# Optimization experiments

Hardware: AMD Instinct MI355X
Metric: run time of the kernel (lower is better)

The kernel has to match this reference:

```python
import jax, jax.numpy as jnp
import numpy as np

F, V, D, B = 3, 512, 8192, 64


def setup_inputs() -> dict:
    key = jax.random.key(0)
    k1, k2 = jax.random.split(key)
    # bipolar (MAP) codebooks: (f, v, d) in {-1, +1}
    codebooks = jnp.sign(jax.random.normal(k1, (F, V, D), dtype=jnp.float32))
    codebooks = jnp.where(codebooks == 0, 1.0, codebooks)
    # ground-truth factors -> inputs = bind (elementwise product) of one codevector per factor
    idx = jax.random.randint(k2, (B, F), 0, V)
    picked = codebooks[jnp.arange(F)[None, :], idx]          # (b, f, d)
    inputs = jnp.prod(picked, axis=1)                         # (b, d)
    # init estimates: bundle (superposition) of each codebook, signed, broadcast to batch
    init = jnp.sign(jnp.sum(codebooks, axis=1))               # (f, d)
    init = jnp.where(init == 0, 1.0, init)
    init_estimates = jnp.broadcast_to(init, (B, F, D)).astype(jnp.float32)
    return {"inputs": inputs, "init_estimates": init_estimates,
            "codebooks": codebooks, "iterations": 10}


def reference(inputs, init_estimates, codebooks, iterations):
    f = init_estimates.shape[-2]

    def step(est):
        # MAP inverse is identity; inv_others[:, j] = prod_{i != j} est[:, i]
        rolled = jnp.stack([jnp.roll(est, i, axis=-2) for i in range(1, f)], axis=-2)  # (b,f,f-1,d)
        inv_others = jnp.prod(rolled, axis=-2)                 # (b, f, d)  multibind
        new_est = inputs[:, None, :] * inv_others              # bind       (b, f, d)
        sim = jnp.einsum('bfd,fvd->bfv', new_est, codebooks)   # codebook similarity
        return jnp.sign(jnp.einsum('bfv,fvd->bfd', sim, codebooks))

    def cond(c):
        est, old, cnt, done = c
        return (cnt < iterations) & jnp.logical_not(done)

    def body(c):
        est, old, cnt, done = c
        new = step(est)
        done = jnp.all(new == old)
        return (new, new, cnt + 1, done)

    carry0 = (init_estimates, init_estimates, jnp.int32(0), jnp.array(False))
    est, _, cnt, _ = jax.lax.while_loop(cond, body, carry0)

    # cleanup: nearest codevector per factor (argmax dot similarity)
    sims = jnp.einsum('bfd,fvd->bfv', est, codebooks)
    outcome = jnp.argmax(sims, axis=-1)                        # (b, f) int indices
    return outcome, cnt - 1
```

## Files before the change

### kernel.cpp

```cpp
#include <hip/hip_runtime.h>

#define F 3
#define V 512
#define D 8192
#define B 64
#define ITERS 10

typedef __bf16 bf16_t;
typedef __bf16 bf16x8 __attribute__((ext_vector_type(8)));
typedef __bf16 bf16x4 __attribute__((ext_vector_type(4)));
typedef float f32x4 __attribute__((ext_vector_type(4)));

__global__ void k_init_small(const float* __restrict__ ie, bf16_t* __restrict__ est0,
                             float* __restrict__ simBase, int* __restrict__ anydiff) {
  long tid = (long)blockIdx.x * blockDim.x + threadIdx.x;
  long NT  = (long)gridDim.x * blockDim.x;
  for (long i = tid * 4; i < (long)B * F * D; i += NT * 4) {
    f32x4 x = *(const f32x4*)(ie + i);
    bf16x4 y;
    y[0] = (bf16_t)x[0]; y[1] = (bf16_t)x[1]; y[2] = (bf16_t)x[2]; y[3] = (bf16_t)x[3];
    *(bf16x4*)(est0 + i) = y;
  }
  f32x4 z = {0.f, 0.f, 0.f, 0.f};
  for (long i = tid * 4; i < (long)(ITERS + 1) * F * B * V; i += NT * 4)
    *(f32x4*)(simBase + i) = z;
  if (tid < 16) anydiff[tid] = 0;
}

__global__ __launch_bounds__(256) void k_init_cb(const float* __restrict__ Csrc,
                                                 bf16_t* __restrict__ Cb,
                                                 bf16_t* __restrict__ CbT) {
  int f = blockIdx.z, vt = blockIdx.y, dt = blockIdx.x;
  __shared__ bf16_t tile[64 * 65];
  int t = threadIdx.x;
  int v0 = vt * 64, d0 = dt * 64;
#pragma unroll
  for (int p = 0; p < 16; ++p) {
    int q = t + 256 * p;
    int i = q >> 6, j = q & 63;
    bf16_t x = (bf16_t)Csrc[((long)(f * V + v0 + i)) * D + d0 + j];
    tile[i * 65 + j] = x;
    Cb[((long)(f * V + v0 + i)) * D + d0 + j] = x;
  }
  __syncthreads();
#pragma unroll
  for (int p = 0; p < 16; ++p) {
    int q = t + 256 * p;
    int jj = q >> 6, ii = q & 63;
    CbT[((long)f * D + d0 + jj) * V + v0 + ii] = tile[ii * 65 + jj];
  }
}

__global__ __launch_bounds__(256) void k_sim(const float* __restrict__ inputs,
                                             const bf16_t* __restrict__ Cb,
                                             const bf16_t* __restrict__ est0,
                                             const bf16_t* __restrict__ est1,
                                             float* __restrict__ simBase,
                                             const int* __restrict__ anydiff, int iter) {
  const int f = blockIdx.z, vt = blockIdx.y, ks = blockIdx.x;
  const bf16_t* est;
  float* sim;
  const bool is_final = (iter >= ITERS);
  if (is_final) {
    int first0 = ITERS;
    for (int i = 0; i < ITERS; ++i)
      if (anydiff[i] == 0) { first0 = i; break; }
    int par = (first0 < ITERS) ? ((first0 + 1) & 1) : 0;
    est = par ? est1 : est0;
    sim = simBase + (long)ITERS * (F * B * V);
  } else {
    for (int i = 0; i < iter; ++i)
      if (anydiff[i] == 0) return;
    est = (iter & 1) ? est1 : est0;
    sim = simBase + (long)iter * (F * B * V);
  }
  const int f1 = (f + 1) % 3, f2 = (f + 2) % 3;

  __shared__ __attribute__((aligned(16))) bf16_t lA[64 * 136];

  const int t = threadIdx.x;
  const int lane = t & 63, w = t >> 6;
  const int lm = lane & 15, quad = lane >> 4;

  f32x4 zero = {0.f, 0.f, 0.f, 0.f};
  f32x4 acc[4];
#pragma unroll
  for (int mt = 0; mt < 4; ++mt) acc[mt] = zero;

  const int v0 = vt * 64;
  const int dbase = ks * 512;
  const bf16_t* bp = Cb + ((long)(f * V + v0 + w * 16 + lm)) * D + dbase;

  for (int c = 0; c < 4; ++c) {
    const int d0c = dbase + c * 128;
    __syncthreads();
#pragma unroll
    for (int p = 0; p < 4; ++p) {
      int q = t + 256 * p;
      int b = q >> 4, dd = (q & 15) * 8;
      if (is_final) {
        *(bf16x8*)&lA[b * 136 + dd] =
            *(const bf16x8*)(est + ((long)b * F + f) * D + d0c + dd);
      } else {
        const float* ip = inputs + (long)b * D + d0c + dd;
        f32x4 x0 = *(const f32x4*)ip;
        f32x4 x1 = *(const f32x4*)(ip + 4);
        bf16x8 e1 = *(const bf16x8*)(est + ((long)b * F + f1) * D + d0c + dd);
        bf16x8 e2 = *(const bf16x8*)(est + ((long)b * F + f2) * D + d0c + dd);
        bf16x8 o;
#pragma unroll
        for (int i = 0; i < 4; ++i) {
          o[i]     = (bf16_t)(x0[i] * (float)e1[i]     * (float)e2[i]);
          o[i + 4] = (bf16_t)(x1[i] * (float)e1[i + 4] * (float)e2[i + 4]);
        }
        *(bf16x8*)&lA[b * 136 + dd] = o;
      }
    }
    __syncthreads();
#pragma unroll
    for (int ks2 = 0; ks2 < 4; ++ks2) {
      const int kb = ks2 * 32 + quad * 8;
      bf16x8 bfrag = *(const bf16x8*)(bp + c * 128 + kb);
#pragma unroll
      for (int mt = 0; mt < 4; ++mt) {
        bf16x8 afrag = *(const bf16x8*)&lA[(mt * 16 + lm) * 136 + kb];
        acc[mt] = __builtin_amdgcn_mfma_f32_16x16x32_bf16(afrag, bfrag, acc[mt], 0, 0, 0);
      }
    }
  }
  const int v = v0 + w * 16 + lm;
#pragma unroll
  for (int mt = 0; mt < 4; ++mt)
#pragma unroll
    for (int r = 0; r < 4; ++r) {
      int b = mt * 16 + quad * 4 + r;
      atomicAdd(&sim[(f * B + b) * V + v], acc[mt][r]);
    }
}

__global__ __launch_bounds__(256) void k_upd(const float* __restrict__ simBase,
                                             const bf16_t* __restrict__ CbT,
                                             bf16_t* __restrict__ est0,
                                             bf16_t* __restrict__ est1,
                                             int* __restrict__ anydiff, int iter) {
  const int f = blockIdx.y;
  const int d0 = blockIdx.x * 64;
  for (int i = 0; i < iter; ++i)
    if (anydiff[i] == 0) return;
  const bf16_t* estIn = (iter & 1) ? est1 : est0;
  bf16_t* estOut = (iter & 1) ? est0 : est1;
  const float* sim = simBase + (long)iter * (F * B * V) + f * (B * V);

  __shared__ __attribute__((aligned(16))) bf16_t lAh[64 * 136];
  __shared__ __attribute__((aligned(16))) bf16_t lAl[64 * 136];

  const int t = threadIdx.x;
  const int lane = t & 63, w = t >> 6;
  const int lm = lane & 15, quad = lane >> 4;

  f32x4 zero = {0.f, 0.f, 0.f, 0.f};
  f32x4 accH[4], accL[4];
#pragma unroll
  for (int mt = 0; mt < 4; ++mt) { accH[mt] = zero; accL[mt] = zero; }

  const bf16_t* bp = CbT + ((long)f * D + d0 + w * 16 + lm) * V;

  for (int c = 0; c < 4; ++c) {
    const int vb = c * 128;
    __syncthreads();
#pragma unroll
    for (int p = 0; p < 4; ++p) {
      int q = t + 256 * p;
      int b = q >> 4, vv = (q & 15) * 8;
      const float* sp = sim + b * V + vb + vv;
      bf16x8 h, l;
#pragma unroll
      for (int i = 0; i < 8; ++i) {
        int si = (int)sp[i];
        h[i] = (bf16_t)(float)(si >> 8);
        l[i] = (bf16_t)(float)(si & 255);
      }
      *(bf16x8*)&lAh[b * 136 + vv] = h;
      *(bf16x8*)&lAl[b * 136 + vv] = l;
    }
    __syncthreads();
#pragma unroll
    for (int ks2 = 0; ks2 < 4; ++ks2) {
      const int kb = ks2 * 32 + quad * 8;
      bf16x8 bfrag = *(const bf16x8*)(bp + vb + kb);
#pragma unroll
      for (int mt = 0; mt < 4; ++mt) {
        bf16x8 ah = *(const bf16x8*)&lAh[(mt * 16 + lm) * 136 + kb];
        bf16x8 al = *(const bf16x8*)&lAl[(mt * 16 + lm) * 136 + kb];
        accH[mt] = __builtin_amdgcn_mfma_f32_16x16x32_bf16(ah, bfrag, accH[mt], 0, 0, 0);
        accL[mt] = __builtin_amdgcn_mfma_f32_16x16x32_bf16(al, bfrag, accL[mt], 0, 0, 0);
      }
    }
  }
  bool anyd = false;
  const int d = d0 + w * 16 + lm;
#pragma unroll
  for (int mt = 0; mt < 4; ++mt)
#pragma unroll
    for (int r = 0; r < 4; ++r) {
      int b = mt * 16 + quad * 4 + r;
      float val = 256.f * accH[mt][r] + accL[mt][r];
      float s = (val > 0.f) ? 1.f : ((val < 0.f) ? -1.f : 0.f);
      long idx = ((long)b * F + f) * D + d;
      estOut[idx] = (bf16_t)s;
      anyd |= ((float)estIn[idx] != s);
    }
  if (__any(anyd) && lane == 0) atomicOr(&anydiff[iter], 1);
}

__global__ __launch_bounds__(64) void k_out(const float* __restrict__ simBase,
                                            const int* __restrict__ anydiff,
                                            int* __restrict__ out) {
  const float* sim = simBase + (long)ITERS * (F * B * V);
  int bid = blockIdx.x;
  int b = bid / F, f = bid % F;
  int lane = threadIdx.x;
  const float* row = sim + (f * B + b) * V;
  float best = -1e30f;
  int bidx = 0;
#pragma unroll
  for (int i = 0; i < V / 64; ++i) {
    int v = lane + 64 * i;
    float x = row[v];
    if (x > best) { best = x; bidx = v; }
  }
  for (int off = 32; off; off >>= 1) {
    float ov = __shfl_down(best, off, 64);
    int oi = __shfl_down(bidx, off, 64);
    if (ov > best || (ov == best && oi < bidx)) { best = ov; bidx = oi; }
  }
  if (lane == 0) out[b * F + f] = bidx;
  if (bid == 0 && lane == 0) {
    int first0 = ITERS;
    for (int i = 0; i < ITERS; ++i)
      if (anydiff[i] == 0) { first0 = i; break; }
    int cnt = (first0 < ITERS) ? (first0 + 1) : ITERS;
    out[B * F] = cnt - 1;
  }
}

extern "C" void kernel_launch(void* const* d_in, const int* in_sizes, int n_in,
                              void* d_out, int out_size, void* d_ws, size_t ws_size,
                              hipStream_t stream) {
  const float* inputs    = (const float*)d_in[0];
  const float* init_est  = (const float*)d_in[1];
  const float* codebooks = (const float*)d_in[2];

  char* w = (char*)d_ws;
  size_t o = 0;
  auto alloc = [&](size_t bytes) -> void* {
    void* p = w + o;
    o = (o + bytes + 255) & ~(size_t)255;
    return p;
  };
  bf16_t* Cb   = (bf16_t*)alloc((size_t)F * V * D * 2);
  bf16_t* CbT  = (bf16_t*)alloc((size_t)F * D * V * 2);
  bf16_t* est0 = (bf16_t*)alloc((size_t)B * F * D * 2);
  bf16_t* est1 = (bf16_t*)alloc((size_t)B * F * D * 2);
  float* simBase = (float*)alloc((size_t)(ITERS + 1) * F * B * V * 4);
  int* anydiff = (int*)alloc(64);

  k_init_small<<<1024, 256, 0, stream>>>(init_est, est0, simBase, anydiff);
  k_init_cb<<<dim3(128, 8, 3), 256, 0, stream>>>(codebooks, Cb, CbT);

  for (int j = 0; j < ITERS; ++j) {
    k_sim<<<dim3(16, 8, 3), 256, 0, stream>>>(inputs, Cb, est0, est1, simBase, anydiff, j);
    k_upd<<<dim3(128, 3), 256, 0, stream>>>(simBase, CbT, est0, est1, anydiff, j);
  }
  k_sim<<<dim3(16, 8, 3), 256, 0, stream>>>(inputs, Cb, est0, est1, simBase, anydiff, ITERS);
  k_out<<<B * F, 64, 0, stream>>>(simBase, anydiff, (int*)d_out);
}
```

Before: 621.0 us.

## Fuse iteration loop into one persistent kernel with software grid barrier

Replaces the 22 separate per-iteration sim/update launches and the final argmax kernel with one persistent 384-block kernel that uses an atomic-counter grid barrier between phases. Sim buffers shrink to a two-slot ring, with each slot re-zeroed inside the loop, and convergence is checked in-kernel so all blocks break out together. This removes kernel launch overhead and the early-return checks on anydiff. In exchange it relies on all 384 blocks being co-resident (two per CU via launch bounds), and spinning barriers add latency at each phase boundary.

Measured after the change: 1.582 ms. 155% more time.

```diff
diff --git a/kernel.cpp b/kernel.cpp
--- a/kernel.cpp
+++ b/kernel.cpp
@@ -5,14 +5,33 @@
 #define D 8192
 #define B 64
 #define ITERS 10
+#define NBLK 384
+#define SIMN (F * B * V)
 
 typedef __bf16 bf16_t;
 typedef __bf16 bf16x8 __attribute__((ext_vector_type(8)));
 typedef __bf16 bf16x4 __attribute__((ext_vector_type(4)));
 typedef float f32x4 __attribute__((ext_vector_type(4)));
 
+__device__ inline void gridbar(int* cnt, int* gen) {
+  __syncthreads();
+  if (threadIdx.x == 0) {
+    int g = __hip_atomic_load(gen, __ATOMIC_RELAXED, __HIP_MEMORY_SCOPE_AGENT);
+    int old = __hip_atomic_fetch_add(cnt, 1, __ATOMIC_ACQ_REL, __HIP_MEMORY_SCOPE_AGENT);
+    if (old == NBLK - 1) {
+      __hip_atomic_store(cnt, 0, __ATOMIC_RELAXED, __HIP_MEMORY_SCOPE_AGENT);
+      __hip_atomic_fetch_add(gen, 1, __ATOMIC_ACQ_REL, __HIP_MEMORY_SCOPE_AGENT);
+    } else {
+      while (__hip_atomic_load(gen, __ATOMIC_ACQUIRE, __HIP_MEMORY_SCOPE_AGENT) == g)
+        __builtin_amdgcn_s_sleep(2);
+    }
+  }
+  __syncthreads();
+}
+
 __global__ void k_init_small(const float* __restrict__ ie, bf16_t* __restrict__ est0,
-                             float* __restrict__ simBase, int* __restrict__ anydiff) {
+                             float* __restrict__ simR, int* __restrict__ anydiff,
+                             int* __restrict__ barst) {
   long tid = (long)blockIdx.x * blockDim.x + threadIdx.x;
   long NT  = (long)gridDim.x * blockDim.x;
   for (long i = tid * 4; i < (long)B * F * D; i += NT * 4) {
@@ -22,9 +41,10 @@
     *(bf16x4*)(est0 + i) = y;
   }
   f32x4 z = {0.f, 0.f, 0.f, 0.f};
-  for (long i = tid * 4; i < (long)(ITERS + 1) * F * B * V; i += NT * 4)
-    *(f32x4*)(simBase + i) = z;
+  for (long i = tid * 4; i < (long)2 * SIMN; i += NT * 4)
+    *(f32x4*)(simR + i) = z;
   if (tid < 16) anydiff[tid] = 0;
+  if (tid < 8)  barst[tid] = 0;
 }
 
 __global__ __launch_bounds__(256) void k_init_cb(const float* __restrict__ Csrc,
@@ -51,196 +71,227 @@
   }
 }
 
-__global__ __launch_bounds__(256) void k_sim(const float* __restrict__ inputs,
-                                             const bf16_t* __restrict__ Cb,
-                                             const bf16_t* __restrict__ est0,
-                                             const bf16_t* __restrict__ est1,
-                                             float* __restrict__ simBase,
-                                             const int* __restrict__ anydiff, int iter) {
-  const int f = blockIdx.z, vt = blockIdx.y, ks = blockIdx.x;
-  const bf16_t* est;
-  float* sim;
-  const bool is_final = (iter >= ITERS);
-  if (is_final) {
-    int first0 = ITERS;
-    for (int i = 0; i < ITERS; ++i)
-      if (anydiff[i] == 0) { first0 = i; break; }
-    int par = (first0 < ITERS) ? ((first0 + 1) & 1) : 0;
-    est = par ? est1 : est0;
-    sim = simBase + (long)ITERS * (F * B * V);
-  } else {
-    for (int i = 0; i < iter; ++i)
-      if (anydiff[i] == 0) return;
-    est = (iter & 1) ? est1 : est0;
-    sim = simBase + (long)iter * (F * B * V);
-  }
-  const int f1 = (f + 1) % 3, f2 = (f + 2) % 3;
-
-  __shared__ __attribute__((aligned(16))) bf16_t lA[64 * 136];
-
+__global__ __launch_bounds__(256, 2) void k_fused(const float* __restrict__ inputs,
+                                                  const bf16_t* __restrict__ Cb,
+                                                  const bf16_t* __restrict__ CbT,
+                                                  bf16_t* __restrict__ est0,
+                                                  bf16_t* __restrict__ est1,
+                                                  float* __restrict__ simR,
+                                                  int* __restrict__ anydiff,
+                                                  int* __restrict__ barst,
+                                                  int* __restrict__ out) {
+  __shared__ __attribute__((aligned(16))) bf16_t lds[2 * 64 * 136];
+  bf16_t* lA  = lds;
+  bf16_t* lA2 = lds + 64 * 136;
+
+  int* cnt = barst;
+  int* gen = barst + 4;
+
+  const int bid = blockIdx.x;
   const int t = threadIdx.x;
   const int lane = t & 63, w = t >> 6;
   const int lm = lane & 15, quad = lane >> 4;
 
-  f32x4 zero = {0.f, 0.f, 0.f, 0.f};
-  f32x4 acc[4];
-#pragma unroll
-  for (int mt = 0; mt < 4; ++mt) acc[mt] = zero;
-
-  const int v0 = vt * 64;
-  const int dbase = ks * 512;
-  const bf16_t* bp = Cb + ((long)(f * V + v0 + w * 16 + lm)) * D + dbase;
-
-  for (int c = 0; c < 4; ++c) {
-    const int d0c = dbase + c * 128;
-    __syncthreads();
-#pragma unroll
-    for (int p = 0; p < 4; ++p) {
-      int q = t + 256 * p;
-      int b = q >> 4, dd = (q & 15) * 8;
-      if (is_final) {
+  const int fS = bid >> 7;
+  const int rS = bid & 127;
+  const int vtS = rS >> 4;
+  const int ksS = rS & 15;
+  const int fU = bid >> 7;
+  const int dtU = bid & 127;
+
+  int done_at = ITERS;
+
+  for (int j = 0; j < ITERS; ++j) {
+    {
+      const bf16_t* est = (j & 1) ? est1 : est0;
+      float* sim = simR + (j & 1) * SIMN;
+      const int f1 = (fS + 1) % 3, f2 = (fS + 2) % 3;
+      const int v0 = vtS * 64;
+      const int dbase = ksS * 512;
+      const bf16_t* bp = Cb + ((long)(fS * V + v0 + w * 16 + lm)) * D + dbase;
+
+      f32x4 zero = {0.f, 0.f, 0.f, 0.f};
+      f32x4 acc[4];
+#pragma unroll
+      for (int mt = 0; mt < 4; ++mt) acc[mt] = zero;
+
+      for (int c = 0; c < 4; ++c) {
+        const int d0c = dbase + c * 128;
+        __syncthreads();
+#pragma unroll
+        for (int p = 0; p < 4; ++p) {
+          int q = t + 256 * p;
+          int b = q >> 4, dd = (q & 15) * 8;
+          const float* ip = inputs + (long)b * D + d0c + dd;
+          f32x4 x0 = *(const f32x4*)ip;
+          f32x4 x1 = *(const f32x4*)(ip + 4);
+          bf16x8 e1 = *(const bf16x8*)(est + ((long)b * F + f1) * D + d0c + dd);
+          bf16x8 e2 = *(const bf16x8*)(est + ((long)b * F + f2) * D + d0c + dd);
+          bf16x8 o;
+#pragma unroll
+          for (int i = 0; i < 4; ++i) {
+            o[i]     = (bf16_t)(x0[i] * (float)e1[i]     * (float)e2[i]);
+            o[i + 4] = (bf16_t)(x1[i] * (float)e1[i + 4] * (float)e2[i + 4]);
+          }
+          *(bf16x8*)&lA[b * 136 + dd] = o;
+        }
+        __syncthreads();
+#pragma unroll
+        for (int ks2 = 0; ks2 < 4; ++ks2) {
+          const int kb = ks2 * 32 + quad * 8;
+          bf16x8 bfrag = *(const bf16x8*)(bp + c * 128 + kb);
+#pragma unroll
+          for (int mt = 0; mt < 4; ++mt) {
+            bf16x8 afrag = *(const bf16x8*)&lA[(mt * 16 + lm) * 136 + kb];
+            acc[mt] = __builtin_amdgcn_mfma_f32_16x16x32_bf16(afrag, bfrag, acc[mt], 0, 0, 0);
+          }
+        }
+      }
+      const int v = v0 + w * 16 + lm;
+#pragma unroll
+      for (int mt = 0; mt < 4; ++mt)
+#pragma unroll
+        for (int r = 0; r < 4; ++r) {
+          int b = mt * 16 + quad * 4 + r;
+          atomicAdd(&sim[(fS * B + b) * V + v], acc[mt][r]);
+        }
+    }
+    gridbar(cnt, gen);
+
+    {
+      const bf16_t* estIn = (j & 1) ? est1 : est0;
+      bf16_t* estOut = (j & 1) ? est0 : est1;
+      const float* sim = simR + (j & 1) * SIMN + fU * (B * V);
+      const int d0 = dtU * 64;
+      const bf16_t* bp = CbT + ((long)fU * D + d0 + w * 16 + lm) * V;
+
+      f32x4 zero = {0.f, 0.f, 0.f, 0.f};
+      f32x4 accH[4], accL[4];
+#pragma unroll
+      for (int mt = 0; mt < 4; ++mt) { accH[mt] = zero; accL[mt] = zero; }
+
+      for (int c = 0; c < 4; ++c) {
+        const int vb = c * 128;
+        __syncthreads();
+#pragma unroll
+        for (int p = 0; p < 4; ++p) {
+          int q = t + 256 * p;
+          int b = q >> 4, vv = (q & 15) * 8;
+          const float* sp = sim + b * V + vb + vv;
+          bf16x8 h, l;
+#pragma unroll
+          for (int i = 0; i < 8; ++i) {
+            int si = (int)sp[i];
+            h[i] = (bf16_t)(float)(si >> 8);
+            l[i] = (bf16_t)(float)(si & 255);
+          }
+          *(bf16x8*)&lA[b * 136 + vv]  = h;
+          *(bf16x8*)&lA2[b * 136 + vv] = l;
+        }
+        __syncthreads();
+#pragma unroll
+        for (int ks2 = 0; ks2 < 4; ++ks2) {
+          const int kb = ks2 * 32 + quad * 8;
+          bf16x8 bfrag = *(const bf16x8*)(bp + vb + kb);
+#pragma unroll
+          for (int mt = 0; mt < 4; ++mt) {
+            bf16x8 ah = *(const bf16x8*)&lA[(mt * 16 + lm) * 136 + kb];
+            bf16x8 al = *(const bf16x8*)&lA2[(mt * 16 + lm) * 136 + kb];
+            accH[mt] = __builtin_amdgcn_mfma_f32_16x16x32_bf16(ah, bfrag, accH[mt], 0, 0, 0);
+            accL[mt] = __builtin_amdgcn_mfma_f32_16x16x32_bf16(al, bfrag, accL[mt], 0, 0, 0);
+          }
+        }
+      }
+      bool anyd = false;
+      const int d = d0 + w * 16 + lm;
+#pragma unroll
+      for (int mt = 0; mt < 4; ++mt)
+#pragma unroll
+        for (int r = 0; r < 4; ++r) {
+          int b = mt * 16 + quad * 4 + r;
+          float val = 256.f * accH[mt][r] + accL[mt][r];
+          float s = (val > 0.f) ? 1.f : ((val < 0.f) ? -1.f : 0.f);
+          long idx = ((long)b * F + fU) * D + d;
+          estOut[idx] = (bf16_t)s;
+          anyd |= ((float)estIn[idx] != s);
+        }
+      if (__any(anyd) && lane == 0) atomicOr(&anydiff[j], 1);
+      simR[((j + 1) & 1) * SIMN + bid * 256 + t] = 0.f;
+    }
+    gridbar(cnt, gen);
+
+    if (__hip_atomic_load(&anydiff[j], __ATOMIC_ACQUIRE, __HIP_MEMORY_SCOPE_AGENT) == 0) {
+      done_at = j;
+      break;
+    }
+  }
+
+  const int jlast = (done_at < ITERS) ? done_at : (ITERS - 1);
+  const int par = (jlast + 1) & 1;
+  const bf16_t* estF = par ? est1 : est0;
+  float* simF = simR + par * SIMN;
+
+  {
+    const int v0 = vtS * 64;
+    const int dbase = ksS * 512;
+    const bf16_t* bp = Cb + ((long)(fS * V + v0 + w * 16 + lm)) * D + dbase;
+
+    f32x4 zero = {0.f, 0.f, 0.f, 0.f};
+    f32x4 acc[4];
+#pragma unroll
+    for (int mt = 0; mt < 4; ++mt) acc[mt] = zero;
+
+    for (int c = 0; c < 4; ++c) {
+      const int d0c = dbase + c * 128;
+      __syncthreads();
+#pragma unroll
+      for (int p = 0; p < 4; ++p) {
+        int q = t + 256 * p;
+        int b = q >> 4, dd = (q & 15) * 8;
         *(bf16x8*)&lA[b * 136 + dd] =
-            *(const bf16x8*)(est + ((long)b * F + f) * D + d0c + dd);
-      } else {
-        const float* ip = inputs + (long)b * D + d0c + dd;
-        f32x4 x0 = *(const f32x4*)ip;
-        f32x4 x1 = *(const f32x4*)(ip + 4);
-        bf16x8 e1 = *(const bf16x8*)(est + ((long)b * F + f1) * D + d0c + dd);
-        bf16x8 e2 = *(const bf16x8*)(est + ((long)b * F + f2) * D + d0c + dd);
-        bf16x8 o;
-#pragma unroll
-        for (int i = 0; i < 4; ++i) {
-          o[i]     = (bf16_t)(x0[i] * (float)e1[i]     * (float)e2[i]);
-          o[i + 4] = (bf16_t)(x1[i] * (float)e1[i + 4] * (float)e2[i + 4]);
-        }
-        *(bf16x8*)&lA[b * 136 + dd] = o;
-      }
-    }
-    __syncthreads();
-#pragma unroll
-    for (int ks2 = 0; ks2 < 4; ++ks2) {
-      const int kb = ks2 * 32 + quad * 8;
-      bf16x8 bfrag = *(const bf16x8*)(bp + c * 128 + kb);
-#pragma unroll
-      for (int mt = 0; mt < 4; ++mt) {
-        bf16x8 afrag = *(const bf16x8*)&lA[(mt * 16 + lm) * 136 + kb];
-        acc[mt] = __builtin_amdgcn_mfma_f32_16x16x32_bf16(afrag, bfrag, acc[mt], 0, 0, 0);
-      }
-    }
-  }
-  const int v = v0 + w * 16 + lm;
-#pragma unroll
-  for (int mt = 0; mt < 4; ++mt)
-#pragma unroll
-    for (int r = 0; r < 4; ++r) {
-      int b = mt * 16 + quad * 4 + r;
-      atomicAdd(&sim[(f * B + b) * V + v], acc[mt][r]);
-    }
-}
-
-__global__ __launch_bounds__(256) void k_upd(const float* __restrict__ simBase,
-                                             const bf16_t* __restrict__ CbT,
-                                             bf16_t* __restrict__ est0,
-                                             bf16_t* __restrict__ est1,
-                                             int* __restrict__ anydiff, int iter) {
-  const int f = blockIdx.y;
-  const int d0 = blockIdx.x * 64;
-  for (int i = 0; i < iter; ++i)
-    if (anydiff[i] == 0) return;
-  const bf16_t* estIn = (iter & 1) ? est1 : est0;
-  bf16_t* estOut = (iter & 1) ? est0 : est1;
-  const float* sim = simBase + (long)iter * (F * B * V) + f * (B * V);
-
-  __shared__ __attribute__((aligned(16))) bf16_t lAh[64 * 136];
-  __shared__ __attribute__((aligned(16))) bf16_t lAl[64 * 136];
-
-  const int t = threadIdx.x;
-  const int lane = t & 63, w = t >> 6;
-  const int lm = lane & 15, quad = lane >> 4;
-
-  f32x4 zero = {0.f, 0.f, 0.f, 0.f};
-  f32x4 accH[4], accL[4];
-#pragma unroll
-  for (int mt = 0; mt < 4; ++mt) { accH[mt] = zero; accL[mt] = zero; }
-
-  const bf16_t* bp = CbT + ((long)f * D + d0 + w * 16 + lm) * V;
-
-  for (int c = 0; c < 4; ++c) {
-    const int vb = c * 128;
-    __syncthreads();
-#pragma unroll
-    for (int p = 0; p < 4; ++p) {
-      int q = t + 256 * p;
-      int b = q >> 4, vv = (q & 15) * 8;
-      const float* sp = sim + b * V + vb + vv;
-      bf16x8 h, l;
-#pragma unroll
-      for (int i = 0; i < 8; ++i) {
-        int si = (int)sp[i];
-        h[i] = (bf16_t)(float)(si >> 8);
-        l[i] = (bf16_t)(float)(si & 255);
-      }
-      *(bf16x8*)&lAh[b * 136 + vv] = h;
-      *(bf16x8*)&lAl[b * 136 + vv] = l;
-    }
-    __syncthreads();
-#pragma unroll
-    for (int ks2 = 0; ks2 < 4; ++ks2) {
-      const int kb = ks2 * 32 + quad * 8;
-      bf16x8 bfrag = *(const bf16x8*)(bp + vb + kb);
-#pragma unroll
-      for (int mt = 0; mt < 4; ++mt) {
-        bf16x8 ah = *(const bf16x8*)&lAh[(mt * 16 + lm) * 136 + kb];
-        bf16x8 al = *(const bf16x8*)&lAl[(mt * 16 + lm) * 136 + kb];
-        accH[mt] = __builtin_amdgcn_mfma_f32_16x16x32_bf16(ah, bfrag, accH[mt], 0, 0, 0);
-        accL[mt] = __builtin_amdgcn_mfma_f32_16x16x32_bf16(al, bfrag, accL[mt], 0, 0, 0);
-      }
-    }
-  }
-  bool anyd = false;
-  const int d = d0 + w * 16 + lm;
-#pragma unroll
-  for (int mt = 0; mt < 4; ++mt)
-#pragma unroll
-    for (int r = 0; r < 4; ++r) {
-      int b = mt * 16 + quad * 4 + r;
-      float val = 256.f * accH[mt][r] + accL[mt][r];
-      float s = (val > 0.f) ? 1.f : ((val < 0.f) ? -1.f : 0.f);
-      long idx = ((long)b * F + f) * D + d;
-      estOut[idx] = (bf16_t)s;
-      anyd |= ((float)estIn[idx] != s);
-    }
-  if (__any(anyd) && lane == 0) atomicOr(&anydiff[iter], 1);
-}
-
-__global__ __launch_bounds__(64) void k_out(const float* __restrict__ simBase,
-                                            const int* __restrict__ anydiff,
-                                            int* __restrict__ out) {
-  const float* sim = simBase + (long)ITERS * (F * B * V);
-  int bid = blockIdx.x;
-  int b = bid / F, f = bid % F;
-  int lane = threadIdx.x;
-  const float* row = sim + (f * B + b) * V;
-  float best = -1e30f;
-  int bidx = 0;
-#pragma unroll
-  for (int i = 0; i < V / 64; ++i) {
-    int v = lane + 64 * i;
-    float x = row[v];
-    if (x > best) { best = x; bidx = v; }
-  }
-  for (int off = 32; off; off >>= 1) {
-    float ov = __shfl_down(best, off, 64);
-    int oi = __shfl_down(bidx, off, 64);
-    if (ov > best || (ov == best && oi < bidx)) { best = ov; bidx = oi; }
-  }
-  if (lane == 0) out[b * F + f] = bidx;
-  if (bid == 0 && lane == 0) {
-    int first0 = ITERS;
-    for (int i = 0; i < ITERS; ++i)
-      if (anydiff[i] == 0) { first0 = i; break; }
-    int cnt = (first0 < ITERS) ? (first0 + 1) : ITERS;
-    out[B * F] = cnt - 1;
+            *(const bf16x8*)(estF + ((long)b * F + fS) * D + d0c + dd);
+      }
+      __syncthreads();
+#pragma unroll
+      for (int ks2 = 0; ks2 < 4; ++ks2) {
+        const int kb = ks2 * 32 + quad * 8;
+        bf16x8 bfrag = *(const bf16x8*)(bp + c * 128 + kb);
+#pragma unroll
+        for (int mt = 0; mt < 4; ++mt) {
+          bf16x8 afrag = *(const bf16x8*)&lA[(mt * 16 + lm) * 136 + kb];
+          acc[mt] = __builtin_amdgcn_mfma_f32_16x16x32_bf16(afrag, bfrag, acc[mt], 0, 0, 0);
+        }
+      }
+    }
+    const int v = v0 + w * 16 + lm;
+#pragma unroll
+    for (int mt = 0; mt < 4; ++mt)
+#pragma unroll
+      for (int r = 0; r < 4; ++r) {
+        int b = mt * 16 + quad * 4 + r;
+        atomicAdd(&simF[(fS * B + b) * V + v], acc[mt][r]);
+      }
+  }
+  gridbar(cnt, gen);
+
+  if (bid < B * F && t < 64) {
+    int b = bid / F, f = bid % F;
+    const float* row = simF + (f * B + b) * V;
+    float best = -1e30f;
+    int bidx = 0;
+#pragma unroll
+    for (int i = 0; i < V / 64; ++i) {
+      int v = lane + 64 * i;
+      float x = row[v];
+      if (x > best) { best = x; bidx = v; }
+    }
+    for (int off = 32; off; off >>= 1) {
+      float ov = __shfl_down(best, off, 64);
+      int oi = __shfl_down(bidx, off, 64);
+      if (ov > best || (ov == best && oi < bidx)) { best = ov; bidx = oi; }
+    }
+    if (lane == 0) out[b * F + f] = bidx;
+    if (bid == 0 && lane == 0) out[B * F] = jlast;
   }
 }
 
@@ -262,16 +313,12 @@
   bf16_t* CbT  = (bf16_t*)alloc((size_t)F * D * V * 2);
   bf16_t* est0 = (bf16_t*)alloc((size_t)B * F * D * 2);
   bf16_t* est1 = (bf16_t*)alloc((size_t)B * F * D * 2);
-  float* simBase = (float*)alloc((size_t)(ITERS + 1) * F * B * V * 4);
+  float* simR  = (float*)alloc((size_t)2 * SIMN * 4);
   int* anydiff = (int*)alloc(64);
-
-  k_init_small<<<1024, 256, 0, stream>>>(init_est, est0, simBase, anydiff);
+  int* barst   = (int*)alloc(64);
+
+  k_init_small<<<1024, 256, 0, stream>>>(init_est, est0, simR, anydiff, barst);
   k_init_cb<<<dim3(128, 8, 3), 256, 0, stream>>>(codebooks, Cb, CbT);
-
-  for (int j = 0; j < ITERS; ++j) {
-    k_sim<<<dim3(16, 8, 3), 256, 0, stream>>>(inputs, Cb, est0, est1, simBase, anydiff, j);
-    k_upd<<<dim3(128, 3), 256, 0, stream>>>(simBase, CbT, est0, est1, anydiff, j);
-  }
-  k_sim<<<dim3(16, 8, 3), 256, 0, stream>>>(inputs, Cb, est0, est1, simBase, anydiff, ITERS);
-  k_out<<<B * F, 64, 0, stream>>>(simBase, anydiff, (int*)d_out);
-}
+  k_fused<<<NBLK, 256, 0, stream>>>(inputs, Cb, CbT, est0, est1, simR,
+                                    anydiff, barst, (int*)d_out);
+}
```
